# Kernel tuning notes

Measured on AMD Instinct MI355X. Metric: run time of the kernel, lower is better.

The kernel has to match this reference:

```python
import jax, jax.numpy as jnp
import numpy as np

D = 512   # word_dim
H = 4     # heads
NEG = -1.0e9


def setup_inputs() -> dict:
    key = jax.random.key(0)
    ks = jax.random.split(key, 9)
    B, N, K = 4, 1024, 32
    neibor_embedding = jax.random.normal(ks[0], (B, N, K, D), dtype=jnp.float32)
    x = jax.random.normal(ks[1], (B, N, D), dtype=jnp.float32)
    mask = jax.random.randint(ks[2], (B, N, K), 0, 2, dtype=jnp.int32)
    s = 1.0 / np.sqrt(D)
    Wq = jax.random.normal(ks[3], (D, D), dtype=jnp.float32) * s
    bq = jax.random.normal(ks[4], (D,), dtype=jnp.float32) * s
    Wk = jax.random.normal(ks[5], (D, D), dtype=jnp.float32) * s
    bk = jax.random.normal(ks[6], (D,), dtype=jnp.float32) * s
    Wv = jax.random.normal(ks[7], (D, D), dtype=jnp.float32) * s
    bv = jax.random.normal(ks[8], (D,), dtype=jnp.float32) * s
    return {"neibor_embedding": neibor_embedding, "mask": mask, "x": x,
            "Wq": Wq, "bq": bq, "Wk": Wk, "bk": bk, "Wv": Wv, "bv": bv}


def reference(neibor_embedding, mask, x, Wq, bq, Wk, bk, Wv, bv):
    B, N, K, Dm = neibor_embedding.shape
    dh = Dm // H
    # torch Linear: y = x @ W.T + b
    q = x @ Wq.T + bq                        # [B, N, D]
    k = neibor_embedding @ Wk.T + bk         # [B, N, K, D]
    v = neibor_embedding @ Wv.T + bv         # [B, N, K, D]
    q = q.reshape(B, N, H, dh)
    k = k.reshape(B, N, K, H, dh)
    v = v.reshape(B, N, K, H, dh)
    # broadcast q*k sum over head_dim -> scores [B, N, H, K] (no 1/sqrt(d) scaling, per source)
    scores = jnp.einsum('bnhd,bnkhd->bnhk', q, k)
    m = (mask[:, :, None, :] == 0)           # [B, N, 1, K] broadcasts over heads
    scores = jnp.where(m, NEG, scores)
    attn = jax.nn.softmax(scores, axis=3)    # [B, N, H, K]
    vec = jnp.einsum('bnhk,bnkhd->bnhd', attn, v)  # [B, N, H, dh]
    return vec.reshape(B, N, Dm)
```

## Files before the change

### kernel.cpp

```cpp
#include <hip/hip_runtime.h>

#define DD   512
#define KK_N 32
#define HH   4
#define DH   128
#define BN_TOT 4096

template<bool BT, int BM, int BN, int TM, int TN, int ZBITS>
__global__ __launch_bounds__(256)
void sgemm(const float* __restrict__ A, int lda, int bA1, int bA0,
           const float* __restrict__ B, int ldb, int bB1, int bB0,
           float* __restrict__ C, int ldc, int bC1, int bC0,
           int Kd)
{
    constexpr int BK = 16;
    constexpr int KG = BK / 4;
    constexpr int A_LOADS = (BM * BK) / (4 * 256);
    constexpr int B_LOADS = (BN * BK) / (4 * 256);
    constexpr int NTX = BN / TN;

    const int zlo = blockIdx.z & ((1 << ZBITS) - 1);
    const int zhi = blockIdx.z >> ZBITS;
    A += (long)zhi * bA1 + (long)zlo * bA0;
    B += (long)zhi * bB1 + (long)zlo * bB0;
    C += (long)zhi * bC1 + (long)zlo * bC0;

    __shared__ __align__(16) float As[BK][BM + 4];
    __shared__ __align__(16) float Bs[BK][BN + 4];

    const int t  = threadIdx.x;
    const int tx = t % NTX;
    const int ty = t / NTX;
    const int rbase = blockIdx.y * BM;
    const int obase = blockIdx.x * BN;

    float4 av[A_LOADS], bv[B_LOADS];
    auto loadAB = [&](int k0) {
#pragma unroll
        for (int i = 0; i < A_LOADS; i++) {
            int s = t + i * 256, row = s / KG, kg = s % KG;
            av[i] = *(const float4*)&A[(long)(rbase + row) * lda + k0 + kg * 4];
        }
#pragma unroll
        for (int i = 0; i < B_LOADS; i++) {
            int s = t + i * 256;
            if (BT) {
                int row = s / KG, kg = s % KG;
                bv[i] = *(const float4*)&B[(long)(obase + row) * ldb + k0 + kg * 4];
            } else {
                int kr = s / (BN / 4), oc = s % (BN / 4);
                bv[i] = *(const float4*)&B[(long)(k0 + kr) * ldb + obase + oc * 4];
            }
        }
    };

    float acc[TM][TN] = {};
    loadAB(0);

    for (int k0 = 0; k0 < Kd; k0 += BK) {
        __syncthreads();
#pragma unroll
        for (int i = 0; i < A_LOADS; i++) {
            int s = t + i * 256, row = s / KG, kg = s % KG;
            const float* ap = (const float*)&av[i];
#pragma unroll
            for (int j = 0; j < 4; j++) As[kg * 4 + j][row] = ap[j];
        }
#pragma unroll
        for (int i = 0; i < B_LOADS; i++) {
            int s = t + i * 256;
            if (BT) {
                int row = s / KG, kg = s % KG;
                const float* bp = (const float*)&bv[i];
#pragma unroll
                for (int j = 0; j < 4; j++) Bs[kg * 4 + j][row] = bp[j];
            } else {
                int kr = s / (BN / 4), oc = s % (BN / 4);
                *(float4*)&Bs[kr][oc * 4] = bv[i];
            }
        }
        __syncthreads();
        if (k0 + BK < Kd) loadAB(k0 + BK);
#pragma unroll
        for (int kk = 0; kk < BK; kk++) {
            float a[TM], b[TN];
#pragma unroll
            for (int im = 0; im < TM / 4; im++) {
                float4 v = *(const float4*)&As[kk][ty * TM + im * 4];
                a[im*4+0] = v.x; a[im*4+1] = v.y; a[im*4+2] = v.z; a[im*4+3] = v.w;
            }
#pragma unroll
            for (int in = 0; in < TN / 4; in++) {
                float4 v = *(const float4*)&Bs[kk][tx * TN + in * 4];
                b[in*4+0] = v.x; b[in*4+1] = v.y; b[in*4+2] = v.z; b[in*4+3] = v.w;
            }
#pragma unroll
            for (int i = 0; i < TM; i++)
#pragma unroll
                for (int j = 0; j < TN; j++)
                    acc[i][j] = fmaf(a[i], b[j], acc[i][j]);
        }
    }

#pragma unroll
    for (int i = 0; i < TM; i++) {
#pragma unroll
        for (int in = 0; in < TN / 4; in++) {
            float4 o;
            o.x = acc[i][in*4+0];
            o.y = acc[i][in*4+1];
            o.z = acc[i][in*4+2];
            o.w = acc[i][in*4+3];
            *(float4*)&C[(long)(rbase + ty * TM + i) * ldc + obase + tx * TN + in * 4] = o;
        }
    }
}

__global__ __launch_bounds__(256)
void add2_bias(const float4* __restrict__ a, const float4* __restrict__ b,
               const float4* __restrict__ bias, float4* __restrict__ o, int n4)
{
    for (int i = blockIdx.x * 256 + threadIdx.x; i < n4; i += gridDim.x * 256) {
        float4 va = a[i], vb = b[i], vc = bias[i & 127];
        float4 r;
        r.x = va.x + vb.x + vc.x;
        r.y = va.y + vb.y + vc.y;
        r.z = va.z + vb.z + vc.z;
        r.w = va.w + vb.w + vc.w;
        o[i] = r;
    }
}

__global__ __launch_bounds__(256)
void attn_fused(const float* __restrict__ ne,
                const int*   __restrict__ mask,
                const float* __restrict__ q,
                const float* g,
                const float* __restrict__ bk,
                float* wne)
{
    const int bn   = blockIdx.x;
    const int t    = threadIdx.x;
    const int wave = t >> 6;
    const int lane = t & 63;

    __shared__ __align__(16) float ne_s[16][516];
    __shared__ __align__(16) float g_s[HH * DD];
    __shared__ float part[4][16][HH];
    __shared__ float p_s[HH][16];
    __shared__ float c_s[HH];
    __shared__ float m_s[HH], l_s[HH], alpha_s[HH];

    {
        const float4* gs = (const float4*)(g + (long)bn * (HH * DD));
        float4 v0 = gs[t];
        float4 v1 = gs[t + 256];
        *(float4*)&g_s[t * 4]         = v0;
        *(float4*)&g_s[(t + 256) * 4] = v1;
    }
    {
        float2 q2 = *(const float2*)&q[(long)bn * DD + wave * DH + lane * 2];
        float2 b2 = *(const float2*)&bk[wave * DH + lane * 2];
        float cp = q2.x * b2.x + q2.y * b2.y;
#pragma unroll
        for (int off = 32; off >= 1; off >>= 1)
            cp += __shfl_xor(cp, off, 64);
        if (lane == 0) c_s[wave] = cp;
    }
    if (t < HH) { m_s[t] = -__builtin_inff(); l_s[t] = 0.f; }

    float wacc[8] = {};
    const int h_own = t >> 6;
    const int d8    = (t & 63) * 8;
    const int kk    = t & 15;
    const int rep   = t >> 4;

    for (int ch = 0; ch < 2; ch++) {
        __syncthreads();
        {
            const float4* src = (const float4*)(ne + (long)bn * (KK_N * DD) + ch * (16 * DD));
#pragma unroll
            for (int i = 0; i < 8; i++) {
                int f = i * 256 + t;
                float4 v = src[f];
                *(float4*)&ne_s[f >> 7][(f & 127) * 4] = v;
            }
        }
        __syncthreads();
        {
            float acc[HH] = {};
#pragma unroll
            for (int i = 0; i < 8; i++) {
                float4 nv = *(const float4*)&ne_s[kk][rep * 32 + i * 4];
#pragma unroll
                for (int h = 0; h < HH; h++) {
                    float4 gv = *(const float4*)&g_s[h * DD + rep * 32 + i * 4];
                    acc[h] = fmaf(nv.x, gv.x, acc[h]);
                    acc[h] = fmaf(nv.y, gv.y, acc[h]);
                    acc[h] = fmaf(nv.z, gv.z, acc[h]);
                    acc[h] = fmaf(nv.w, gv.w, acc[h]);
                }
            }
#pragma unroll
            for (int h = 0; h < HH; h++) {
                acc[h] += __shfl_xor(acc[h], 16, 64);
                acc[h] += __shfl_xor(acc[h], 32, 64);
            }
            if ((t & 48) == 0) {
#pragma unroll
                for (int h = 0; h < HH; h++) part[wave][kk][h] = acc[h];
            }
        }
        __syncthreads();
        if (t < 64) {
            int k_i = t & 15, h = t >> 4;
            float s = part[0][k_i][h] + part[1][k_i][h] + part[2][k_i][h]
                    + part[3][k_i][h] + c_s[h];
            if (mask[(long)bn * KK_N + ch * 16 + k_i] == 0) s = -1.0e9f;
            float mx = s;
#pragma unroll
            for (int off = 8; off >= 1; off >>= 1)
                mx = fmaxf(mx, __shfl_xor(mx, off, 64));
            float m_old = m_s[h];
            float m_new = fmaxf(m_old, mx);
            float p = expf(s - m_new);
            float sm = p;
#pragma unroll
            for (int off = 8; off >= 1; off >>= 1)
                sm += __shfl_xor(sm, off, 64);
            p_s[h][k_i] = p;
            if (k_i == 0) {
                float alpha = expf(m_old - m_new);
                alpha_s[h] = alpha;
                l_s[h] = l_s[h] * alpha + sm;
                m_s[h] = m_new;
            }
        }
        __syncthreads();
        {
            float alpha = alpha_s[h_own];
#pragma unroll
            for (int j = 0; j < 8; j++) wacc[j] *= alpha;
#pragma unroll
            for (int k2 = 0; k2 < 16; k2++) {
                float pk = p_s[h_own][k2];
                float4 n0 = *(const float4*)&ne_s[k2][d8];
                float4 n1 = *(const float4*)&ne_s[k2][d8 + 4];
                wacc[0] = fmaf(pk, n0.x, wacc[0]);
                wacc[1] = fmaf(pk, n0.y, wacc[1]);
                wacc[2] = fmaf(pk, n0.z, wacc[2]);
                wacc[3] = fmaf(pk, n0.w, wacc[3]);
                wacc[4] = fmaf(pk, n1.x, wacc[4]);
                wacc[5] = fmaf(pk, n1.y, wacc[5]);
                wacc[6] = fmaf(pk, n1.z, wacc[6]);
                wacc[7] = fmaf(pk, n1.w, wacc[7]);
            }
        }
    }
    float rl = 1.0f / l_s[h_own];
    float4 o0 = make_float4(wacc[0] * rl, wacc[1] * rl, wacc[2] * rl, wacc[3] * rl);
    float4 o1 = make_float4(wacc[4] * rl, wacc[5] * rl, wacc[6] * rl, wacc[7] * rl);
    float* dst = wne + (long)bn * (HH * DD) + t * 8;
    *(float4*)&dst[0] = o0;
    *(float4*)&dst[4] = o1;
}

extern "C" void kernel_launch(void* const* d_in, const int* in_sizes, int n_in,
                              void* d_out, int out_size, void* d_ws, size_t ws_size,
                              hipStream_t stream) {
    (void)in_sizes; (void)n_in; (void)out_size; (void)ws_size;
    const float* ne  = (const float*)d_in[0];
    const int*   msk = (const int*)  d_in[1];
    const float* x   = (const float*)d_in[2];
    const float* Wq  = (const float*)d_in[3];
    const float* bq  = (const float*)d_in[4];
    const float* Wk  = (const float*)d_in[5];
    const float* bk  = (const float*)d_in[6];
    const float* Wv  = (const float*)d_in[7];
    const float* bv  = (const float*)d_in[8];
    float* out = (float*)d_out;

    const long NQ = (long)BN_TOT * DD;
    float* q_ws  = (float*)d_ws;
    float* g_ws  = q_ws + NQ;
    float* qpart = g_ws + (long)BN_TOT * HH * DD;
    float* opart = qpart + 2 * NQ;

    dim3 blk(256);
    sgemm<true, 128, 64, 8, 4, 1><<<dim3(8, 32, 2), blk, 0, stream>>>(
        x, DD, 0, 256, Wq, DD, 0, 256, qpart, DD, 0, (int)NQ, 256);
    add2_bias<<<dim3(512), blk, 0, stream>>>(
        (const float4*)qpart, (const float4*)(qpart + NQ),
        (const float4*)bq, (float4*)q_ws, (int)(NQ / 4));
    sgemm<false, 128, 128, 8, 8, 0><<<dim3(4, 32, HH), blk, 0, stream>>>(
        q_ws, DD, DH, 0, Wk, DD, DH * DD, 0, g_ws, HH * DD, DD, 0, DH);
    attn_fused<<<dim3(BN_TOT), blk, 0, stream>>>(ne, msk, q_ws, g_ws, bk, g_ws);
    sgemm<true, 128, 64, 8, 4, 1><<<dim3(2, 32, 2 * HH), blk, 0, stream>>>(
        g_ws, HH * DD, DD, 256, Wv, DD, DH * DD, 256, opart, DD, DH, (int)NQ, 256);
    add2_bias<<<dim3(512), blk, 0, stream>>>(
        (const float4*)opart, (const float4*)(opart + NQ),
        (const float4*)bv, (float4*)out, (int)(NQ / 4));
}
```

Before: 487.0 us.

## Replace FP32 SIMT GEMMs with split-bf16 MFMA GEMMs and fused bias epilogue

Replaces the three FP32 CUDA-core style sgemm launches with a bf16x3 (hi/lo split) MFMA GEMM that approximates FP32 accuracy using matrix cores, and folds the bias add into the GEMM epilogue. This removes the split-K partial buffers and the two add2_bias kernels. Wk is pre-transposed by a small kernel so every GEMM uses the same B-transposed layout. The split-bf16 scheme drops the lo*lo term and adds per-tile conversion work in shared-memory staging. The output stores are scalar rather than vectorized.

```diff
diff --git a/kernel.cpp b/kernel.cpp
--- a/kernel.cpp
+++ b/kernel.cpp
@@ -6,128 +6,153 @@
 #define DH   128
 #define BN_TOT 4096
 
-template<bool BT, int BM, int BN, int TM, int TN, int ZBITS>
+typedef __bf16 bf16x8 __attribute__((ext_vector_type(8)));
+typedef float  f32x4  __attribute__((ext_vector_type(4)));
+
+__device__ __forceinline__ unsigned rne_bf16(float x) {
+    unsigned u = __float_as_uint(x);
+    return (u + 0x7fffu + ((u >> 16) & 1u)) >> 16;
+}
+
 __global__ __launch_bounds__(256)
-void sgemm(const float* __restrict__ A, int lda, int bA1, int bA0,
-           const float* __restrict__ B, int ldb, int bB1, int bB0,
-           float* __restrict__ C, int ldc, int bC1, int bC0,
-           int Kd)
+void prep_wkT(const float* __restrict__ Wk, float* __restrict__ WkT)
 {
-    constexpr int BK = 16;
-    constexpr int KG = BK / 4;
-    constexpr int A_LOADS = (BM * BK) / (4 * 256);
-    constexpr int B_LOADS = (BN * BK) / (4 * 256);
-    constexpr int NTX = BN / TN;
-
-    const int zlo = blockIdx.z & ((1 << ZBITS) - 1);
-    const int zhi = blockIdx.z >> ZBITS;
-    A += (long)zhi * bA1 + (long)zlo * bA0;
-    B += (long)zhi * bB1 + (long)zlo * bB0;
-    C += (long)zhi * bC1 + (long)zlo * bC0;
-
-    __shared__ __align__(16) float As[BK][BM + 4];
-    __shared__ __align__(16) float Bs[BK][BN + 4];
-
-    const int t  = threadIdx.x;
-    const int tx = t % NTX;
-    const int ty = t / NTX;
+    __shared__ float tile[32][DH + 1];
+    const int h = blockIdx.y, o0 = blockIdx.x * 32, t = threadIdx.x;
+#pragma unroll
+    for (int r = 0; r < 16; r++) {
+        int k = (t >> 5) + r * 8;
+        tile[t & 31][k] = Wk[(long)(h * DH + k) * DD + o0 + (t & 31)];
+    }
+    __syncthreads();
+#pragma unroll
+    for (int r = 0; r < 16; r++) {
+        int ol = (t >> 7) + r * 2;
+        WkT[((long)h * DD + o0 + ol) * DH + (t & 127)] = tile[ol][t & 127];
+    }
+}
+
+template<int BM, int BN>
+__global__ __launch_bounds__(256)
+void gemm_bf16x2(const float* __restrict__ A, int lda, long sA,
+                 const float* __restrict__ B, int ldb, long sB,
+                 float*       __restrict__ C, int ldc, long sC,
+                 const float* __restrict__ bias, int sBias,
+                 int Kd)
+{
+    constexpr int BK  = 64;
+    constexpr int LDW = 2 * BK + 8;
+    constexpr int A_LOADS = BM * BK / 1024;
+    constexpr int B_LOADS = BN * BK / 1024;
+    constexpr int WM = BM / 2, WN = BN / 2;
+    constexpr int MI = WM / 16, NI = WN / 16;
+
+    const int z = blockIdx.z;
+    A += (long)z * sA;
+    B += (long)z * sB;
+    C += (long)z * sC;
+    if (bias) bias += (long)z * sBias;
+
+    __shared__ __align__(16) unsigned short As[BM * LDW];
+    __shared__ __align__(16) unsigned short Bs[BN * LDW];
+
+    const int t    = threadIdx.x;
+    const int lane = t & 63;
+    const int wave = t >> 6;
+    const int wm   = wave >> 1, wn = wave & 1;
     const int rbase = blockIdx.y * BM;
     const int obase = blockIdx.x * BN;
 
-    float4 av[A_LOADS], bv[B_LOADS];
+    float4 areg[A_LOADS], breg[B_LOADS];
     auto loadAB = [&](int k0) {
 #pragma unroll
         for (int i = 0; i < A_LOADS; i++) {
-            int s = t + i * 256, row = s / KG, kg = s % KG;
-            av[i] = *(const float4*)&A[(long)(rbase + row) * lda + k0 + kg * 4];
+            int s = t + i * 256, k4 = s & 15, row = s >> 4;
+            areg[i] = *(const float4*)&A[(long)(rbase + row) * lda + k0 + k4 * 4];
         }
 #pragma unroll
         for (int i = 0; i < B_LOADS; i++) {
-            int s = t + i * 256;
-            if (BT) {
-                int row = s / KG, kg = s % KG;
-                bv[i] = *(const float4*)&B[(long)(obase + row) * ldb + k0 + kg * 4];
-            } else {
-                int kr = s / (BN / 4), oc = s % (BN / 4);
-                bv[i] = *(const float4*)&B[(long)(k0 + kr) * ldb + obase + oc * 4];
-            }
+            int s = t + i * 256, k4 = s & 15, row = s >> 4;
+            breg[i] = *(const float4*)&B[(long)(obase + row) * ldb + k0 + k4 * 4];
         }
     };
-
-    float acc[TM][TN] = {};
+    auto cvt_store = [&](unsigned short* dst, float4 v, int row, int k4) {
+        unsigned h0 = rne_bf16(v.x), h1 = rne_bf16(v.y);
+        unsigned h2 = rne_bf16(v.z), h3 = rne_bf16(v.w);
+        float l0 = v.x - __uint_as_float(h0 << 16);
+        float l1 = v.y - __uint_as_float(h1 << 16);
+        float l2 = v.z - __uint_as_float(h2 << 16);
+        float l3 = v.w - __uint_as_float(h3 << 16);
+        int off = row * LDW + (k4 >> 1) * 16 + (k4 & 1) * 4;
+        uint2 hw = make_uint2(h0 | (h1 << 16), h2 | (h3 << 16));
+        uint2 lw = make_uint2(rne_bf16(l0) | (rne_bf16(l1) << 16),
+                              rne_bf16(l2) | (rne_bf16(l3) << 16));
+        *(uint2*)&dst[off]     = hw;
+        *(uint2*)&dst[off + 8] = lw;
+    };
+
+    f32x4 acc[MI][NI];
+#pragma unroll
+    for (int m = 0; m < MI; m++)
+#pragma unroll
+        for (int n = 0; n < NI; n++)
+            acc[m][n] = (f32x4){0.f, 0.f, 0.f, 0.f};
+
+    const int a_base = (wm * WM + (lane & 15)) * LDW + (lane >> 4) * 16;
+    const int b_base = (wn * WN + (lane & 15)) * LDW + (lane >> 4) * 16;
+
     loadAB(0);
-
     for (int k0 = 0; k0 < Kd; k0 += BK) {
         __syncthreads();
 #pragma unroll
-        for (int i = 0; i < A_LOADS; i++) {
-            int s = t + i * 256, row = s / KG, kg = s % KG;
-            const float* ap = (const float*)&av[i];
-#pragma unroll
-            for (int j = 0; j < 4; j++) As[kg * 4 + j][row] = ap[j];
-        }
-#pragma unroll
-        for (int i = 0; i < B_LOADS; i++) {
-            int s = t + i * 256;
-            if (BT) {
-                int row = s / KG, kg = s % KG;
-                const float* bp = (const float*)&bv[i];
-#pragma unroll
-                for (int j = 0; j < 4; j++) Bs[kg * 4 + j][row] = bp[j];
-            } else {
-                int kr = s / (BN / 4), oc = s % (BN / 4);
-                *(float4*)&Bs[kr][oc * 4] = bv[i];
-            }
-        }
+        for (int i = 0; i < A_LOADS; i++) { int s = t + i * 256; cvt_store(As, areg[i], s >> 4, s & 15); }
+#pragma unroll
+        for (int i = 0; i < B_LOADS; i++) { int s = t + i * 256; cvt_store(Bs, breg[i], s >> 4, s & 15); }
         __syncthreads();
         if (k0 + BK < Kd) loadAB(k0 + BK);
-#pragma unroll
-        for (int kk = 0; kk < BK; kk++) {
-            float a[TM], b[TN];
-#pragma unroll
-            for (int im = 0; im < TM / 4; im++) {
-                float4 v = *(const float4*)&As[kk][ty * TM + im * 4];
-                a[im*4+0] = v.x; a[im*4+1] = v.y; a[im*4+2] = v.z; a[im*4+3] = v.w;
-            }
-#pragma unroll
-            for (int in = 0; in < TN / 4; in++) {
-                float4 v = *(const float4*)&Bs[kk][tx * TN + in * 4];
-                b[in*4+0] = v.x; b[in*4+1] = v.y; b[in*4+2] = v.z; b[in*4+3] = v.w;
-            }
-#pragma unroll
-            for (int i = 0; i < TM; i++)
-#pragma unroll
-                for (int j = 0; j < TN; j++)
-                    acc[i][j] = fmaf(a[i], b[j], acc[i][j]);
-        }
-    }
-
-#pragma unroll
-    for (int i = 0; i < TM; i++) {
-#pragma unroll
-        for (int in = 0; in < TN / 4; in++) {
-            float4 o;
-            o.x = acc[i][in*4+0];
-            o.y = acc[i][in*4+1];
-            o.z = acc[i][in*4+2];
-            o.w = acc[i][in*4+3];
-            *(float4*)&C[(long)(rbase + ty * TM + i) * ldc + obase + tx * TN + in * 4] = o;
-        }
-    }
-}
-
-__global__ __launch_bounds__(256)
-void add2_bias(const float4* __restrict__ a, const float4* __restrict__ b,
-               const float4* __restrict__ bias, float4* __restrict__ o, int n4)
-{
-    for (int i = blockIdx.x * 256 + threadIdx.x; i < n4; i += gridDim.x * 256) {
-        float4 va = a[i], vb = b[i], vc = bias[i & 127];
-        float4 r;
-        r.x = va.x + vb.x + vc.x;
-        r.y = va.y + vb.y + vc.y;
-        r.z = va.z + vb.z + vc.z;
-        r.w = va.w + vb.w + vc.w;
-        o[i] = r;
+
+#pragma unroll
+        for (int ks = 0; ks < 2; ks++) {
+            bf16x8 ah[MI], al[MI], bh[NI], bl[NI];
+#pragma unroll
+            for (int m = 0; m < MI; m++) {
+                ah[m] = *(const bf16x8*)&As[a_base + m * 16 * LDW + ks * 64];
+                al[m] = *(const bf16x8*)&As[a_base + m * 16 * LDW + ks * 64 + 8];
+            }
+#pragma unroll
+            for (int n = 0; n < NI; n++) {
+                bh[n] = *(const bf16x8*)&Bs[b_base + n * 16 * LDW + ks * 64];
+                bl[n] = *(const bf16x8*)&Bs[b_base + n * 16 * LDW + ks * 64 + 8];
+            }
+#pragma unroll
+            for (int m = 0; m < MI; m++)
+#pragma unroll
+                for (int n = 0; n < NI; n++)
+                    acc[m][n] = __builtin_amdgcn_mfma_f32_16x16x32_bf16(ah[m], bh[n], acc[m][n], 0, 0, 0);
+#pragma unroll
+            for (int m = 0; m < MI; m++)
+#pragma unroll
+                for (int n = 0; n < NI; n++)
+                    acc[m][n] = __builtin_amdgcn_mfma_f32_16x16x32_bf16(ah[m], bl[n], acc[m][n], 0, 0, 0);
+#pragma unroll
+            for (int m = 0; m < MI; m++)
+#pragma unroll
+                for (int n = 0; n < NI; n++)
+                    acc[m][n] = __builtin_amdgcn_mfma_f32_16x16x32_bf16(al[m], bh[n], acc[m][n], 0, 0, 0);
+        }
+    }
+
+#pragma unroll
+    for (int n = 0; n < NI; n++) {
+        int col = obase + wn * WN + n * 16 + (lane & 15);
+        float bv_ = bias ? bias[col] : 0.f;
+#pragma unroll
+        for (int m = 0; m < MI; m++) {
+            int row0 = rbase + wm * WM + m * 16 + (lane >> 4) * 4;
+#pragma unroll
+            for (int j = 0; j < 4; j++)
+                C[(long)(row0 + j) * ldc + col] = acc[m][n][j] + bv_;
+        }
     }
 }
 
@@ -280,24 +305,17 @@
     const float* bv  = (const float*)d_in[8];
     float* out = (float*)d_out;
 
-    const long NQ = (long)BN_TOT * DD;
-    float* q_ws  = (float*)d_ws;
-    float* g_ws  = q_ws + NQ;
-    float* qpart = g_ws + (long)BN_TOT * HH * DD;
-    float* opart = qpart + 2 * NQ;
+    float* q_ws = (float*)d_ws;
+    float* g_ws = q_ws + (long)BN_TOT * DD;
+    float* wkT  = g_ws + (long)BN_TOT * HH * DD;
 
     dim3 blk(256);
-    sgemm<true, 128, 64, 8, 4, 1><<<dim3(8, 32, 2), blk, 0, stream>>>(
-        x, DD, 0, 256, Wq, DD, 0, 256, qpart, DD, 0, (int)NQ, 256);
-    add2_bias<<<dim3(512), blk, 0, stream>>>(
-        (const float4*)qpart, (const float4*)(qpart + NQ),
-        (const float4*)bq, (float4*)q_ws, (int)(NQ / 4));
-    sgemm<false, 128, 128, 8, 8, 0><<<dim3(4, 32, HH), blk, 0, stream>>>(
-        q_ws, DD, DH, 0, Wk, DD, DH * DD, 0, g_ws, HH * DD, DD, 0, DH);
+    prep_wkT<<<dim3(16, HH), blk, 0, stream>>>(Wk, wkT);
+    gemm_bf16x2<64, 128><<<dim3(DD / 128, BN_TOT / 64, 1), blk, 0, stream>>>(
+        x, DD, 0, Wq, DD, 0, q_ws, DD, 0, bq, 0, DD);
+    gemm_bf16x2<64, 128><<<dim3(DD / 128, BN_TOT / 64, HH), blk, 0, stream>>>(
+        q_ws, DD, DH, wkT, DH, (long)DD * DH, g_ws, HH * DD, DD, nullptr, 0, DH);
     attn_fused<<<dim3(BN_TOT), blk, 0, stream>>>(ne, msk, q_ws, g_ws, bk, g_ws);
-    sgemm<true, 128, 64, 8, 4, 1><<<dim3(2, 32, 2 * HH), blk, 0, stream>>>(
-        g_ws, HH * DD, DD, 256, Wv, DD, DH * DD, 256, opart, DD, DH, (int)NQ, 256);
-    add2_bias<<<dim3(512), blk, 0, stream>>>(
-        (const float4*)opart, (const float4*)(opart + NQ),
-        (const float4*)bv, (float4*)out, (int)(NQ / 4));
-}
+    gemm_bf16x2<64, 128><<<dim3(1, BN_TOT / 64, HH), blk, 0, stream>>>(
+        g_ws, HH * DD, DD, Wv, DD, (long)DH * DD, out, DD, DH, bv, DH, DD);
+}
```

After: 446.7 us. 1.09x faster.
